# Performance work log

Hardware: AMD Instinct MI355X
Metric: run time of the kernel (lower is better)

The kernel has to match this reference:

```python
import jax, jax.numpy as jnp
import numpy as np
from jax import lax

B, C, L = 64, 12, 2048
KERN = 9
K = 8            # kernels per group
G = 64           # total groups -> divisor 2, _g = 32
_G = G // 2
N_PER = 6        # clip(C//2, 2, 8)
NUM_DIL = int(np.log2((L - 1) / (KERN - 1))) + 1  # 8


def _normalize(W):
    W = W - W.mean(-1, keepdims=True)
    return W / jnp.abs(W).sum(-1, keepdims=True)


def setup_inputs() -> dict:
    key = jax.random.key(0)
    kx, kw, ki = jax.random.split(key, 3)
    X = jax.random.normal(kx, (B, C, L), dtype=jnp.float32)
    W = _normalize(jax.random.normal(kw, (NUM_DIL, 2, K * _G, 1, KERN), dtype=jnp.float32))
    I = jax.random.randint(ki, (NUM_DIL, 2, _G, N_PER), 0, C, dtype=jnp.int32)
    return {"X": X, "W": W, "I": I}


def _branch(src, w, idx, d, p, k, g):
    # src: [B, C, L'], w: [k*g, 1, 9], idx: [g, n_per]
    b = src.shape[0]
    sel = src[:, idx].sum(2)  # [B, g, L'] channel-subset sum
    conv = lax.conv_general_dilated(
        sel, w, window_strides=(1,), padding=[(p, p)], rhs_dilation=(d,),
        dimension_numbers=("NCH", "OIH", "NCH"), feature_group_count=g,
    )  # [B, k*g, L']
    Zc = conv.reshape(b, g, k, -1)
    max_vals = Zc.max(2)            # [B, g, L']
    max_idx = Zc.argmax(2)          # [B, g, L'] in [0, k)
    min_idx = Zc.argmin(2)
    b_ix = jnp.arange(b)[:, None, None]
    g_ix = jnp.arange(g)[None, :, None]
    count_max = jnp.zeros((b, g, k), Zc.dtype).at[b_ix, g_ix, max_idx].add(max_vals)
    count_min = jnp.zeros((b, g, k), Zc.dtype).at[b_ix, g_ix, min_idx].add(1.0)
    return count_max, count_min


def reference(X, W, I):
    b = X.shape[0]
    k = W.shape[2] // I.shape[2]
    g = I.shape[2]
    num_dil = W.shape[0]
    diff_X = jnp.diff(X, axis=-1)
    outs = []
    for di in range(num_dil):
        d = 2 ** di
        p = ((KERN - 1) * d) // 2
        for diff in range(2):
            src = X if diff == 0 else diff_X
            cmax, cmin = _branch(src, W[di, diff], I[di, diff], d, p, k, g)
            outs.append(cmax)
            outs.append(cmin)
    Z = jnp.concatenate(outs, axis=1)  # [B, num_dil*2*2*g, k]
    return Z.reshape(b, -1)
```

## Files before the change

### kernel.cpp

```cpp
#include <hip/hip_runtime.h>
#include <stdint.h>

#define BB     64
#define CC     12
#define LL     2048
#define KERNSZ 9
#define KK     8
#define GG     32
#define NPER   6
#define NDIL   8
#define PAD    256
#define MAIN   2048
#define BUFSZ  (PAD + MAIN + PAD)
#define WPB    4

typedef float f2 __attribute__((ext_vector_type(2)));
typedef float f4 __attribute__((ext_vector_type(4)));

__device__ __forceinline__ void pk_fma_bcast(f2& acc, const f2& t, uint64_t wpair) {
    asm("v_pk_fma_f32 %0, %1, %2, %0 op_sel:[0,0,0] op_sel_hi:[0,1,1]"
        : "+v"(acc) : "v"(t), "s"(wpair));
}
__device__ __forceinline__ f2 pk_mul_bcast(const f2& t, uint64_t wpair) {
    f2 d;
    asm("v_pk_mul_f32 %0, %1, %2 op_sel:[0,0] op_sel_hi:[0,1]"
        : "=v"(d) : "v"(t), "s"(wpair));
    return d;
}

template <int D>
__device__ __forceinline__ void run_phase2(
    const float* __restrict__ sel, int lane, int dif,
    const uint64_t (&wp)[4][KERNSZ], float (&accM)[KK], uint32_t (&accN)[KK])
{
    const float NANF = __uint_as_float(0x7fc00000u);

    #pragma unroll 2
    for (int q = 0; q < 32; ++q) {
        const int pos = q * 64 + lane;

        f2 t[KERNSZ];
        if constexpr (D == 128) {
            #pragma unroll
            for (int j = 0; j < KERNSZ; ++j) {
                int off = pos + (j - 4) * D;
                if (j < 4) off = (off < -PAD) ? -PAD : off;
                if (j > 4) off = (off > MAIN + PAD - 1) ? (MAIN + PAD - 1) : off;
                t[j].x = sel[off];
            }
        } else {
            const float* p = sel + pos - 4 * D;
            #pragma unroll
            for (int j = 0; j < KERNSZ; ++j)
                t[j].x = p[j * D];
        }

        f2 v2[4];
        #pragma unroll
        for (int c = 0; c < 4; ++c)
            v2[c] = pk_mul_bcast(t[0], wp[c][0]);
        #pragma unroll
        for (int j = 1; j < KERNSZ; ++j)
            #pragma unroll
            for (int c = 0; c < 4; ++c)
                pk_fma_bcast(v2[c], t[j], wp[c][j]);

        float v[KK] = { v2[0].x, v2[0].y, v2[1].x, v2[1].y,
                        v2[2].x, v2[2].y, v2[3].x, v2[3].y };

        float m1 = fmaxf(fmaxf(v[0], v[1]), v[2]);
        float m2 = fmaxf(fmaxf(v[3], v[4]), v[5]);
        float m3 = fmaxf(fmaxf(v[6], v[7]), m1);
        float mv = fmaxf(m2, m3);
        float n1 = fminf(fminf(v[0], v[1]), v[2]);
        float n2 = fminf(fminf(v[3], v[4]), v[5]);
        float n3 = fminf(fminf(v[6], v[7]), n1);
        float nv = fminf(n2, n3);

        if (dif && q == 31) {
            if (lane == 63) { mv = NANF; nv = NANF; }
        }

        #pragma unroll
        for (int k = 0; k < KK; ++k) {
            accM[k] += (v[k] == mv) ? v[k] : 0.0f;
            accN[k] += (v[k] == nv) ? 1u : 0u;
        }
    }
}

__global__ __launch_bounds__(256, 4) void hydra_kernel(
    const float* __restrict__ X,
    const float* __restrict__ W,
    const int*   __restrict__ I,
    float*       __restrict__ out)
{
    __shared__ float lds[WPB][BUFSZ];

    const int tid  = threadIdx.x;
    const int wave = tid >> 6;
    const int lane = tid & 63;
    const int wid  = blockIdx.x * WPB + wave;
    const int b   = wid >> 9;
    const int r   = wid & 511;
    const int di  = r >> 6;
    const int r2  = r & 63;
    const int dif = r2 >> 5;
    const int g   = r2 & 31;

    float* buf = lds[wave];
    float* sel = buf + PAD;

    {
        f4 z = {0.0f, 0.0f, 0.0f, 0.0f};
        ((f4*)buf)[lane]                        = z;
        ((f4*)(buf + PAD + MAIN))[lane]         = z;
    }

    const int* Ig = I + ((size_t)((di * 2 + dif) * GG + g)) * NPER;
    const float* xb = X + (size_t)b * CC * LL;
    const f4* c0 = (const f4*)(xb + Ig[0] * LL);
    const f4* c1 = (const f4*)(xb + Ig[1] * LL);
    const f4* c2 = (const f4*)(xb + Ig[2] * LL);
    const f4* c3 = (const f4*)(xb + Ig[3] * LL);
    const f4* c4 = (const f4*)(xb + Ig[4] * LL);
    const f4* c5 = (const f4*)(xb + Ig[5] * LL);
    f4* sel4 = (f4*)sel;

    #pragma unroll 2
    for (int q = 0; q < 8; ++q) {
        int idx = q * 64 + lane;
        f4 s = (c0[idx] + c1[idx]) + (c2[idx] + c3[idx]) + (c4[idx] + c5[idx]);
        sel4[idx] = s;
    }

    if (dif) {
        #pragma unroll 2
        for (int q = 0; q < 8; ++q) {
            int idx = q * 64 + lane;
            f4 a  = sel4[idx];
            float an = sel[idx * 4 + 4];
            f4 v;
            v.x = a.y - a.x;
            v.y = a.z - a.y;
            v.z = a.w - a.z;
            v.w = (idx == 511) ? 0.0f : (an - a.w);
            sel4[idx] = v;
        }
    }

    const float* Wg = W + (size_t)((di * 2 + dif) * (KK * GG) + g * KK) * KERNSZ;
    uint64_t wp[4][KERNSZ];
    #pragma unroll
    for (int c = 0; c < 4; ++c)
        #pragma unroll
        for (int j = 0; j < KERNSZ; ++j) {
            uint32_t lo = __float_as_uint(Wg[(2 * c)     * KERNSZ + j]);
            uint32_t hi = __float_as_uint(Wg[(2 * c + 1) * KERNSZ + j]);
            wp[c][j] = (uint64_t)lo | ((uint64_t)hi << 32);
        }

    float    accM[KK];
    uint32_t accN[KK];
    #pragma unroll
    for (int k = 0; k < KK; ++k) { accM[k] = 0.0f; accN[k] = 0u; }

    switch (di) {
        case 0: run_phase2<1>  (sel, lane, dif, wp, accM, accN); break;
        case 1: run_phase2<2>  (sel, lane, dif, wp, accM, accN); break;
        case 2: run_phase2<4>  (sel, lane, dif, wp, accM, accN); break;
        case 3: run_phase2<8>  (sel, lane, dif, wp, accM, accN); break;
        case 4: run_phase2<16> (sel, lane, dif, wp, accM, accN); break;
        case 5: run_phase2<32> (sel, lane, dif, wp, accM, accN); break;
        case 6: run_phase2<64> (sel, lane, dif, wp, accM, accN); break;
        default: run_phase2<128>(sel, lane, dif, wp, accM, accN); break;
    }

    float* o = out + (size_t)b * 8192 + (size_t)((di * 2 + dif) * 2) * 256 + g * KK;
    #pragma unroll
    for (int k = 0; k < KK; ++k) {
        float a = accM[k];
        unsigned c = accN[k];
        #pragma unroll
        for (int off = 32; off > 0; off >>= 1) {
            a += __shfl_xor(a, off, 64);
            c += __shfl_xor(c, off, 64);
        }
        if (lane == 0) {
            o[k]       = a;
            o[256 + k] = (float)c;
        }
    }
}

extern "C" void kernel_launch(void* const* d_in, const int* in_sizes, int n_in,
                              void* d_out, int out_size, void* d_ws, size_t ws_size,
                              hipStream_t stream) {
    const float* X = (const float*)d_in[0];
    const float* W = (const float*)d_in[1];
    const int*   I = (const int*)d_in[2];
    float* out = (float*)d_out;

    const int total_waves = BB * NDIL * 2 * GG;
    const int blocks = total_waves / WPB;
    hydra_kernel<<<blocks, 256, 0, stream>>>(X, W, I, out);
}
```

Measured before the change: 255.4 us.

## Shrink LDS padding, split clamped edge iterations, use ballot-popcount min counts

Halves the LDS halo padding from 256 to 128 floats per wave. This reduces LDS per block, which could allow more resident waves per CU. Because dilations 64 and 128 now have halos larger than the padding, the position loop is split into clamped prologue/epilogue iterations and an unclamped middle. The min-count accumulation now uses a wave ballot plus popcount into scalar counters instead of per-lane counters, which removes a shuffle reduction. The max/min trees use v_max3/v_min3. In exchange, code size grows and the unrolled edge iterations add register pressure.

```diff
diff --git a/kernel.cpp b/kernel.cpp
--- a/kernel.cpp
+++ b/kernel.cpp
@@ -9,7 +9,7 @@
 #define GG     32
 #define NPER   6
 #define NDIL   8
-#define PAD    256
+#define PAD    128
 #define MAIN   2048
 #define BUFSZ  (PAD + MAIN + PAD)
 #define WPB    4
@@ -27,66 +27,86 @@
         : "=v"(d) : "v"(t), "s"(wpair));
     return d;
 }
+__device__ __forceinline__ float max3f(float a, float b, float c) {
+    float d; asm("v_max3_f32 %0, %1, %2, %3" : "=v"(d) : "v"(a), "v"(b), "v"(c)); return d;
+}
+__device__ __forceinline__ float min3f(float a, float b, float c) {
+    float d; asm("v_min3_f32 %0, %1, %2, %3" : "=v"(d) : "v"(a), "v"(b), "v"(c)); return d;
+}
+
+template <int D, bool CL>
+__device__ __forceinline__ void pos_body(
+    const float* __restrict__ sel, int q, int lane, bool kill,
+    const uint64_t (&wp)[4][KERNSZ], float (&accM)[KK], uint32_t (&cnt)[KK])
+{
+    const int pos = q * 64 + lane;
+
+    f2 t[KERNSZ];
+    #pragma unroll
+    for (int j = 0; j < KERNSZ; ++j) {
+        int off = pos + (j - 4) * D;
+        if constexpr (CL) {
+            off = (off < -PAD) ? -PAD : off;
+            off = (off > MAIN + PAD - 1) ? (MAIN + PAD - 1) : off;
+        }
+        t[j].x = sel[off];
+    }
+
+    f2 v2[4];
+    #pragma unroll
+    for (int c = 0; c < 4; ++c)
+        v2[c] = pk_mul_bcast(t[0], wp[c][0]);
+    #pragma unroll
+    for (int j = 1; j < KERNSZ; ++j)
+        #pragma unroll
+        for (int c = 0; c < 4; ++c)
+            pk_fma_bcast(v2[c], t[j], wp[c][j]);
+
+    float v[KK] = { v2[0].x, v2[0].y, v2[1].x, v2[1].y,
+                    v2[2].x, v2[2].y, v2[3].x, v2[3].y };
+
+    float ma = max3f(v[0], v[1], v[2]);
+    float mb = max3f(v[3], v[4], v[5]);
+    float mc = max3f(v[6], v[7], ma);
+    float mv = fmaxf(mb, mc);
+    float na = min3f(v[0], v[1], v[2]);
+    float nb = min3f(v[3], v[4], v[5]);
+    float nc = min3f(v[6], v[7], na);
+    float nv = fminf(nb, nc);
+
+    if (kill && lane == 63) {
+        const float NANF = __uint_as_float(0x7fc00000u);
+        mv = NANF; nv = NANF;
+    }
+
+    #pragma unroll
+    for (int k = 0; k < KK; ++k) {
+        accM[k] += (v[k] == mv) ? v[k] : 0.0f;
+        cnt[k] += (uint32_t)__popcll(__ballot(v[k] == nv));
+    }
+}
 
 template <int D>
 __device__ __forceinline__ void run_phase2(
     const float* __restrict__ sel, int lane, int dif,
-    const uint64_t (&wp)[4][KERNSZ], float (&accM)[KK], uint32_t (&accN)[KK])
+    const uint64_t (&wp)[4][KERNSZ], float (&accM)[KK], uint32_t (&cnt)[KK])
 {
-    const float NANF = __uint_as_float(0x7fc00000u);
-
+    constexpr int HALO = 4 * D;
+    constexpr bool NEEDCL = (HALO > PAD);
+    constexpr int QLO = NEEDCL ? (HALO - PAD + 63) / 64 : 0;
+    constexpr int QHI = NEEDCL ? (2112 - HALO) / 64 + 1 : 32;
+    constexpr int QMID_END = (QHI < 31) ? QHI : 31;
+
+    #pragma unroll
+    for (int q = 0; q < QLO; ++q)
+        pos_body<D, true>(sel, q, lane, false, wp, accM, cnt);
     #pragma unroll 2
-    for (int q = 0; q < 32; ++q) {
-        const int pos = q * 64 + lane;
-
-        f2 t[KERNSZ];
-        if constexpr (D == 128) {
-            #pragma unroll
-            for (int j = 0; j < KERNSZ; ++j) {
-                int off = pos + (j - 4) * D;
-                if (j < 4) off = (off < -PAD) ? -PAD : off;
-                if (j > 4) off = (off > MAIN + PAD - 1) ? (MAIN + PAD - 1) : off;
-                t[j].x = sel[off];
-            }
-        } else {
-            const float* p = sel + pos - 4 * D;
-            #pragma unroll
-            for (int j = 0; j < KERNSZ; ++j)
-                t[j].x = p[j * D];
-        }
-
-        f2 v2[4];
-        #pragma unroll
-        for (int c = 0; c < 4; ++c)
-            v2[c] = pk_mul_bcast(t[0], wp[c][0]);
-        #pragma unroll
-        for (int j = 1; j < KERNSZ; ++j)
-            #pragma unroll
-            for (int c = 0; c < 4; ++c)
-                pk_fma_bcast(v2[c], t[j], wp[c][j]);
-
-        float v[KK] = { v2[0].x, v2[0].y, v2[1].x, v2[1].y,
-                        v2[2].x, v2[2].y, v2[3].x, v2[3].y };
-
-        float m1 = fmaxf(fmaxf(v[0], v[1]), v[2]);
-        float m2 = fmaxf(fmaxf(v[3], v[4]), v[5]);
-        float m3 = fmaxf(fmaxf(v[6], v[7]), m1);
-        float mv = fmaxf(m2, m3);
-        float n1 = fminf(fminf(v[0], v[1]), v[2]);
-        float n2 = fminf(fminf(v[3], v[4]), v[5]);
-        float n3 = fminf(fminf(v[6], v[7]), n1);
-        float nv = fminf(n2, n3);
-
-        if (dif && q == 31) {
-            if (lane == 63) { mv = NANF; nv = NANF; }
-        }
-
-        #pragma unroll
-        for (int k = 0; k < KK; ++k) {
-            accM[k] += (v[k] == mv) ? v[k] : 0.0f;
-            accN[k] += (v[k] == nv) ? 1u : 0u;
-        }
-    }
+    for (int q = QLO; q < QMID_END; ++q)
+        pos_body<D, false>(sel, q, lane, false, wp, accM, cnt);
+    #pragma unroll
+    for (int q = QMID_END; q < 31; ++q)
+        pos_body<D, true>(sel, q, lane, false, wp, accM, cnt);
+    pos_body<D, NEEDCL>(sel, 31, lane, dif != 0, wp, accM, cnt);
 }
 
 __global__ __launch_bounds__(256, 4) void hydra_kernel(
@@ -112,9 +132,9 @@
     float* sel = buf + PAD;
 
     {
-        f4 z = {0.0f, 0.0f, 0.0f, 0.0f};
-        ((f4*)buf)[lane]                        = z;
-        ((f4*)(buf + PAD + MAIN))[lane]         = z;
+        f2 z = {0.0f, 0.0f};
+        ((f2*)buf)[lane]              = z;
+        ((f2*)(buf + PAD + MAIN))[lane] = z;
     }
 
     const int* Ig = I + ((size_t)((di * 2 + dif) * GG + g)) * NPER;
@@ -161,34 +181,31 @@
         }
 
     float    accM[KK];
-    uint32_t accN[KK];
-    #pragma unroll
-    for (int k = 0; k < KK; ++k) { accM[k] = 0.0f; accN[k] = 0u; }
+    uint32_t cnt[KK];
+    #pragma unroll
+    for (int k = 0; k < KK; ++k) { accM[k] = 0.0f; cnt[k] = 0u; }
 
     switch (di) {
-        case 0: run_phase2<1>  (sel, lane, dif, wp, accM, accN); break;
-        case 1: run_phase2<2>  (sel, lane, dif, wp, accM, accN); break;
-        case 2: run_phase2<4>  (sel, lane, dif, wp, accM, accN); break;
-        case 3: run_phase2<8>  (sel, lane, dif, wp, accM, accN); break;
-        case 4: run_phase2<16> (sel, lane, dif, wp, accM, accN); break;
-        case 5: run_phase2<32> (sel, lane, dif, wp, accM, accN); break;
-        case 6: run_phase2<64> (sel, lane, dif, wp, accM, accN); break;
-        default: run_phase2<128>(sel, lane, dif, wp, accM, accN); break;
+        case 0: run_phase2<1>  (sel, lane, dif, wp, accM, cnt); break;
+        case 1: run_phase2<2>  (sel, lane, dif, wp, accM, cnt); break;
+        case 2: run_phase2<4>  (sel, lane, dif, wp, accM, cnt); break;
+        case 3: run_phase2<8>  (sel, lane, dif, wp, accM, cnt); break;
+        case 4: run_phase2<16> (sel, lane, dif, wp, accM, cnt); break;
+        case 5: run_phase2<32> (sel, lane, dif, wp, accM, cnt); break;
+        case 6: run_phase2<64> (sel, lane, dif, wp, accM, cnt); break;
+        default: run_phase2<128>(sel, lane, dif, wp, accM, cnt); break;
     }
 
     float* o = out + (size_t)b * 8192 + (size_t)((di * 2 + dif) * 2) * 256 + g * KK;
     #pragma unroll
     for (int k = 0; k < KK; ++k) {
         float a = accM[k];
-        unsigned c = accN[k];
         #pragma unroll
-        for (int off = 32; off > 0; off >>= 1) {
+        for (int off = 32; off > 0; off >>= 1)
             a += __shfl_xor(a, off, 64);
-            c += __shfl_xor(c, off, 64);
-        }
         if (lane == 0) {
             o[k]       = a;
-            o[256 + k] = (float)c;
+            o[256 + k] = (float)cnt[k];
         }
     }
 }
```

After: 369.4 us. +44.6%, slower.
